# Optimization experiments

Hardware: AMD Instinct MI355X
Metric: run time of the kernel (lower is better)

## Reference

```python
import jax, jax.numpy as jnp
import numpy as np

B, S, H, NH, L, V, P = 2, 1024, 768, 12, 4, 32000, 1024
HD = H // NH  # head dim = 64; matches scale_val = hidden/num_heads


def setup_inputs() -> dict:
    key = jax.random.key(0)
    ks = jax.random.split(key, 18)
    sc = 0.02
    n = jax.random.normal
    return {
        "input_ids": jax.random.randint(ks[0], (B, S), 0, V, dtype=jnp.int32),
        "seq_mask": jnp.ones((B, S), jnp.float32),
        "bpe_emb": (n(ks[1], (V, H)) * sc).astype(jnp.float32),
        "pos_emb": (n(ks[2], (P, H)) * sc).astype(jnp.float32),
        "qkv_w": (n(ks[3], (L, H, 3 * H)) * sc).astype(jnp.float32),
        "qkv_b": jnp.zeros((L, 3 * H), jnp.float32),
        "res_w": (n(ks[4], (L, H, H)) * sc).astype(jnp.float32),
        "res_b": jnp.zeros((L, H), jnp.float32),
        "ln1_g": jnp.ones((L, H), jnp.float32),
        "ln1_b": jnp.zeros((L, H), jnp.float32),
        "ff1_w": (n(ks[5], (L, H, 4 * H)) * sc).astype(jnp.float32),
        "ff1_b": jnp.zeros((L, 4 * H), jnp.float32),
        "ff2_w": (n(ks[6], (L, 4 * H, H)) * sc).astype(jnp.float32),
        "ff2_b": jnp.zeros((L, H), jnp.float32),
        "ln2_g": jnp.ones((L, H), jnp.float32),
        "ln2_b": jnp.zeros((L, H), jnp.float32),
        "pred_w": (n(ks[7], (H, V)) * sc).astype(jnp.float32),
    }


def _layer_norm(x, g, b, e=1e-5):
    u = jnp.mean(x, -1, keepdims=True)
    s = jnp.mean((x - u) ** 2, -1, keepdims=True)
    return g * ((x - u) / jnp.sqrt(s + e)) + b


def _attention(x, seq_mask, w_qkv, b_qkv, w_res, b_res):
    qkv = x @ w_qkv + b_qkv                    # [B,S,3H]
    q, k, v = jnp.split(qkv, 3, axis=-1)
    q = q.reshape(B, S, NH, HD)
    k = k.reshape(B, S, NH, HD)
    v = v.reshape(B, S, NH, HD)
    score = jnp.einsum('bqhd,bkhd->bhqk', q, k) / jnp.sqrt(jnp.float32(HD))
    tril = jnp.tril(jnp.ones((S, S), jnp.float32))           # causal
    mask = tril[None, None] * seq_mask[:, None, None, :]      # [B,1,S,S]
    score = score + (1.0 - mask) * -1e9
    prob = jax.nn.softmax(score, axis=-1)      # dropout rate 0 -> identity
    val = jnp.einsum('bhqk,bkhd->bqhd', prob, v).reshape(B, S, H)
    return val @ w_res + b_res                 # dropout rate 0 -> identity


def reference(input_ids, seq_mask, bpe_emb, pos_emb, qkv_w, qkv_b, res_w, res_b,
              ln1_g, ln1_b, ff1_w, ff1_b, ff2_w, ff2_b, ln2_g, ln2_b, pred_w):
    pos_idx = jnp.arange(S)
    h = bpe_emb[input_ids] + pos_emb[pos_idx][None]           # [B,S,H]
    for l in range(L):
        a = _attention(h, seq_mask, qkv_w[l], qkv_b[l], res_w[l], res_b[l])
        h = _layer_norm(h + a, ln1_g[l], ln1_b[l])
        m = (jax.nn.gelu(h @ ff1_w[l] + ff1_b[l], approximate=False)
             @ ff2_w[l] + ff2_b[l])
        h = _layer_norm(h + m, ln2_g[l], ln2_b[l])
    pred_score = h @ pred_w                                   # [B,S,V]
    pred_prob = jax.nn.softmax(pred_score, axis=-1)
    return pred_score, pred_prob
```

## Files before the change

### kernel.cpp

```cpp
#include <hip/hip_runtime.h>
#include <math.h>

#define BB 2
#define SS 1024
#define HH 768
#define NHEAD 12
#define HDIM 64
#define NLAYER 4
#define VV 32000
#define MROWS (BB*SS)

typedef unsigned short u16;
typedef __attribute__((ext_vector_type(8))) short short8;
typedef __attribute__((ext_vector_type(4))) float f32x4;
typedef __attribute__((ext_vector_type(4))) unsigned short u16x4;

__device__ __forceinline__ u16 f2bf(float f) {
    union { float f; unsigned u; } x; x.f = f;
    unsigned r = (x.u + 0x7fff + ((x.u >> 16) & 1)) >> 16;
    return (u16)r;
}
__device__ __forceinline__ float bf2f(u16 b) {
    union { unsigned u; float f; } x; x.u = ((unsigned)b) << 16;
    return x.f;
}

__device__ __forceinline__ void gload_lds16(const u16* g, u16* l) {
    __builtin_amdgcn_global_load_lds((const __attribute__((address_space(1))) void*)g,
                                     (__attribute__((address_space(3))) void*)l, 16, 0, 0);
}

__global__ __launch_bounds__(256) void conv_transpose(
    const float* __restrict__ W, u16* __restrict__ Wt, int K, int N) {
    int l = blockIdx.z;
    W  += (size_t)l * K * N;
    Wt += (size_t)l * K * N;
    __shared__ u16 tile[32][33];
    int k0 = blockIdx.y * 32, n0 = blockIdx.x * 32;
    int t = threadIdx.x;
    int ky = t >> 3, nx = (t & 7) * 4;
    float4 v = *(const float4*)(W + (size_t)(k0 + ky) * N + n0 + nx);
    tile[nx + 0][ky] = f2bf(v.x);
    tile[nx + 1][ky] = f2bf(v.y);
    tile[nx + 2][ky] = f2bf(v.z);
    tile[nx + 3][ky] = f2bf(v.w);
    __syncthreads();
    int nr = t >> 3, kc = (t & 7) * 4;
    u16x4 o;
    o[0] = tile[nr][kc + 0]; o[1] = tile[nr][kc + 1];
    o[2] = tile[nr][kc + 2]; o[3] = tile[nr][kc + 3];
    *(u16x4*)(Wt + (size_t)(n0 + nr) * K + k0 + kc) = o;
}

__global__ void embed_kernel(const int* __restrict__ ids,
                             const float* __restrict__ bpe,
                             const float* __restrict__ pos,
                             float* __restrict__ h, u16* __restrict__ hb) {
    int row = blockIdx.x;
    int s = row % SS;
    int id = ids[row];
    const float4* br = (const float4*)(bpe + (size_t)id * HH);
    const float4* pr = (const float4*)(pos + (size_t)s * HH);
    float4* hr = (float4*)(h + (size_t)row * HH);
    u16x4* hbr = (u16x4*)(hb + (size_t)row * HH);
    int t = threadIdx.x;
    float4 a = br[t], c = pr[t];
    a.x += c.x; a.y += c.y; a.z += c.z; a.w += c.w;
    hr[t] = a;
    u16x4 u; u[0] = f2bf(a.x); u[1] = f2bf(a.y); u[2] = f2bf(a.z); u[3] = f2bf(a.w);
    hbr[t] = u;
}

template<int BM, int ACT, int WF32, int WBF>
__global__ __launch_bounds__(256) void mfma_gemm(
    const u16* __restrict__ A, const u16* __restrict__ Wt,
    const float* __restrict__ bias, float* __restrict__ C,
    u16* __restrict__ Cb, int M, int N, int K) {
    constexpr int MR = (BM >= 128) ? 4 : 2;
    __shared__ u16 As[2 * BM * 64];
    __shared__ u16 Bs[2 * 128 * 64];
    const int tid = threadIdx.x;
    const int lane = tid & 63;
    const int wid = tid >> 6;

    const int nwg = gridDim.x * gridDim.y;
    int id = blockIdx.x + gridDim.x * blockIdx.y;
    int id2 = (nwg & 7) ? id : ((id & 7) * (nwg >> 3) + (id >> 3));
    const int brow = (id2 % gridDim.x) * BM;
    const int bcol = (id2 / gridDim.x) * 128;

    const int wr = (wid >> 1) * (MR * 16);
    const int wc = (wid & 1) * 64;
    f32x4 acc[MR][4] = {};

    const u16* Abase = A + (size_t)brow * K;
    const u16* Bbase = Wt + (size_t)bcol * K;
    const int lrow = lane & 15;
    const int lhi = lane >> 4;

    auto stage = [&](u16* Ad, u16* Bd, int kt) {
#pragma unroll
        for (int c0 = 0; c0 < BM * 8; c0 += 256) {
            int c = c0 + tid;
            int r = c >> 3, s = c & 7;
            gload_lds16(Abase + (size_t)r * K + kt + ((s ^ (r & 7)) * 8), Ad + c * 8);
        }
#pragma unroll
        for (int c0 = 0; c0 < 1024; c0 += 256) {
            int c = c0 + tid;
            int r = c >> 3, s = c & 7;
            gload_lds16(Bbase + (size_t)r * K + kt + ((s ^ (r & 7)) * 8), Bd + c * 8);
        }
    };

    const int nt = K / 64;
    stage(As, Bs, 0);
    for (int t = 0; t < nt; ++t) {
        u16* Ac = As + (t & 1) * (BM * 64);
        u16* Bc = Bs + (t & 1) * (128 * 64);
        if (t + 1 < nt) {
            stage(As + ((t + 1) & 1) * (BM * 64),
                  Bs + ((t + 1) & 1) * (128 * 64), (t + 1) * 64);
            if constexpr (BM == 128)      asm volatile("s_waitcnt vmcnt(8)" ::: "memory");
            else                          asm volatile("s_waitcnt vmcnt(6)" ::: "memory");
        } else {
            asm volatile("s_waitcnt vmcnt(0)" ::: "memory");
        }
        __builtin_amdgcn_s_barrier();
        __builtin_amdgcn_sched_barrier(0);

        short8 a[MR][2], b[4][2];
#pragma unroll
        for (int m = 0; m < MR; ++m) {
            const int R = wr + m * 16 + lrow;
            char* rp = (char*)Ac + R * 128;
#pragma unroll
            for (int kk = 0; kk < 2; ++kk)
                a[m][kk] = *(const short8*)(rp + (((kk * 4 + lhi) ^ (R & 7)) * 16));
        }
#pragma unroll
        for (int n = 0; n < 4; ++n) {
            const int R = wc + n * 16 + lrow;
            char* rp = (char*)Bc + R * 128;
#pragma unroll
            for (int kk = 0; kk < 2; ++kk)
                b[n][kk] = *(const short8*)(rp + (((kk * 4 + lhi) ^ (R & 7)) * 16));
        }
        __builtin_amdgcn_s_setprio(1);
#pragma unroll
        for (int kk = 0; kk < 2; ++kk)
#pragma unroll
            for (int m = 0; m < MR; ++m)
#pragma unroll
                for (int n = 0; n < 4; ++n)
                    acc[m][n] = __builtin_amdgcn_mfma_f32_16x16x32_bf16(a[m][kk], b[n][kk], acc[m][n], 0, 0, 0);
        __builtin_amdgcn_s_setprio(0);

        __builtin_amdgcn_sched_barrier(0);
        __builtin_amdgcn_s_barrier();
    }

    const int lr4 = (lane >> 4) * 4;
#pragma unroll
    for (int n = 0; n < 4; ++n) {
        int col = bcol + wc + n * 16 + lrow;
        float bv = bias ? bias[col] : 0.f;
#pragma unroll
        for (int m = 0; m < MR; ++m) {
#pragma unroll
            for (int j = 0; j < 4; ++j) {
                int row = brow + wr + m * 16 + lr4 + j;
                float v = acc[m][n][j] + bv;
                if (ACT == 1) v = 0.5f * v * (1.f + erff(v * 0.70710678118654752f));
                if (WF32) C[(size_t)row * N + col] = v;
                if (WBF)  Cb[(size_t)row * N + col] = f2bf(v);
            }
        }
    }
}

__global__ __launch_bounds__(256) void attn_kernel(
    const u16* __restrict__ qkvb, const float* __restrict__ seq_mask,
    u16* __restrict__ av) {
    __shared__ u16 Ks[64 * 64];
    __shared__ u16 Vt[64 * 64];
    __shared__ u16 Ps[64 * 64];
    const int qb = gridDim.x - 1 - blockIdx.x;
    const int hd = blockIdx.y, b = blockIdx.z;
    const int t = threadIdx.x;
    const int lane = t & 63;
    const int w = t >> 6;
    const int lrow = lane & 15;
    const int lhi = lane >> 4;
    const int q0 = qb * 64;
    const size_t rs = 3 * HH;

    short8 aq[2];
    {
        const u16* qrow = qkvb + (size_t)(b * SS + q0 + w * 16 + lrow) * rs + hd * HDIM;
        aq[0] = *(const short8*)(qrow + lhi * 8);
        aq[1] = *(const short8*)(qrow + 32 + lhi * 8);
    }

    f32x4 o[4] = {};
    float m_[4] = {-INFINITY, -INFINITY, -INFINITY, -INFINITY};
    float l_[4] = {0.f, 0.f, 0.f, 0.f};

    const int kr = t >> 2, dc = t & 3;
    short8 kA, kB, vA, vB;
    {
        const u16* kbase = qkvb + (size_t)(b * SS + kr) * rs + HH + hd * HDIM + dc * 16;
        kA = *(const short8*)(kbase);
        kB = *(const short8*)(kbase + 8);
        vA = *(const short8*)(kbase + HH);
        vB = *(const short8*)(kbase + HH + 8);
    }

    for (int kt = 0; kt <= qb; ++kt) {
        const int k0 = kt * 64;
        __syncthreads();
        {
            char* krowp = (char*)Ks + kr * 128;
            *(short8*)(krowp + (((dc * 32 + 0)  ^ ((kr & 7) << 4)))) = kA;
            *(short8*)(krowp + (((dc * 32 + 16) ^ ((kr & 7) << 4)))) = kB;
#pragma unroll
            for (int e = 0; e < 8; ++e) {
                int d0 = dc * 16 + e;
                int d1 = dc * 16 + 8 + e;
                *(u16*)((char*)Vt + d0 * 128 + ((kr * 2) ^ ((d0 & 7) << 4))) = (u16)vA[e];
                *(u16*)((char*)Vt + d1 * 128 + ((kr * 2) ^ ((d1 & 7) << 4))) = (u16)vB[e];
            }
        }
        __syncthreads();

        if (kt < qb) {
            const u16* kbase = qkvb + (size_t)(b * SS + k0 + 64 + kr) * rs + HH + hd * HDIM + dc * 16;
            kA = *(const short8*)(kbase);
            kB = *(const short8*)(kbase + 8);
            vA = *(const short8*)(kbase + HH);
            vB = *(const short8*)(kbase + HH + 8);
        }

        f32x4 s[4] = {};
        __builtin_amdgcn_s_setprio(1);
#pragma unroll
        for (int n = 0; n < 4; ++n) {
            const int krow = n * 16 + lrow;
            char* kp = (char*)Ks + krow * 128;
#pragma unroll
            for (int c = 0; c < 2; ++c) {
                short8 bk = *(const short8*)(kp + ((c * 64 + lhi * 16) ^ ((krow & 7) << 4)));
                s[n] = __builtin_amdgcn_mfma_f32_16x16x32_bf16(aq[c], bk, s[n], 0, 0, 0);
            }
        }
        __builtin_amdgcn_s_setprio(0);

        float sm[4];
#pragma unroll
        for (int n = 0; n < 4; ++n) sm[n] = seq_mask[b * SS + k0 + n * 16 + lrow];
        const int diag = (kt == qb);
#pragma unroll
        for (int j = 0; j < 4; ++j) {
            const int qglob = q0 + w * 16 + lhi * 4 + j;
            float sv[4];
#pragma unroll
            for (int n = 0; n < 4; ++n) {
                const int kglob = k0 + n * 16 + lrow;
                float msk = (diag && kglob > qglob) ? 0.f : sm[n];
                sv[n] = s[n][j] * 0.125f + (1.f - msk) * (-1e9f);
            }
            float tm = fmaxf(fmaxf(sv[0], sv[1]), fmaxf(sv[2], sv[3]));
            tm = fmaxf(tm, __shfl_xor(tm, 1));
            tm = fmaxf(tm, __shfl_xor(tm, 2));
            tm = fmaxf(tm, __shfl_xor(tm, 4));
            tm = fmaxf(tm, __shfl_xor(tm, 8));
            float mn = fmaxf(m_[j], tm);
            float sc = __expf(m_[j] - mn);
            float ps = 0.f;
#pragma unroll
            for (int n = 0; n < 4; ++n) {
                float p = __expf(sv[n] - mn);
                s[n][j] = p;
                ps += p;
            }
            ps += __shfl_xor(ps, 1);
            ps += __shfl_xor(ps, 2);
            ps += __shfl_xor(ps, 4);
            ps += __shfl_xor(ps, 8);
            l_[j] = l_[j] * sc + ps;
            m_[j] = mn;
#pragma unroll
            for (int dn = 0; dn < 4; ++dn) o[dn][j] *= sc;
        }

#pragma unroll
        for (int j = 0; j < 4; ++j) {
            const int prow = w * 16 + lhi * 4 + j;
            char* pp = (char*)Ps + prow * 128;
#pragma unroll
            for (int n = 0; n < 4; ++n)
                *(u16*)(pp + ((n * 32 + lrow * 2) ^ ((prow & 7) << 4))) = f2bf(s[n][j]);
        }

        const int arow = w * 16 + lrow;
        char* ap_p = (char*)Ps + arow * 128;
        __builtin_amdgcn_s_setprio(1);
#pragma unroll
        for (int c = 0; c < 2; ++c) {
            short8 ap = *(const short8*)(ap_p + ((c * 64 + lhi * 16) ^ ((arow & 7) << 4)));
#pragma unroll
            for (int dn = 0; dn < 4; ++dn) {
                const int vrow = dn * 16 + lrow;
                short8 bv = *(const short8*)((char*)Vt + vrow * 128 +
                                             ((c * 64 + lhi * 16) ^ ((vrow & 7) << 4)));
                o[dn] = __builtin_amdgcn_mfma_f32_16x16x32_bf16(ap, bv, o[dn], 0, 0, 0);
            }
        }
        __builtin_amdgcn_s_setprio(0);
    }

#pragma unroll
    for (int j = 0; j < 4; ++j) {
        const int q = q0 + w * 16 + lhi * 4 + j;
        const float inv = 1.f / l_[j];
        u16* orow = av + (size_t)(b * SS + q) * HH + hd * HDIM;
#pragma unroll
        for (int dn = 0; dn < 4; ++dn)
            orow[dn * 16 + lrow] = f2bf(o[dn][j] * inv);
    }
}

__global__ __launch_bounds__(256) void add_ln_kernel(
    float* __restrict__ h, u16* __restrict__ hb,
    const u16* __restrict__ ab,
    const float* __restrict__ g, const float* __restrict__ bta) {
    const int row = blockIdx.x * 4 + (threadIdx.x >> 6);
    const int lane = threadIdx.x & 63;
    const size_t base = (size_t)row * HH;

    float x[12];
    float sum = 0.f;
#pragma unroll
    for (int c = 0; c < 3; ++c) {
        const int col = lane * 4 + c * 256;
        float4 hv = *(const float4*)(h + base + col);
        u16x4 av = *(const u16x4*)(ab + base + col);
        x[c*4+0] = hv.x + bf2f(av[0]);
        x[c*4+1] = hv.y + bf2f(av[1]);
        x[c*4+2] = hv.z + bf2f(av[2]);
        x[c*4+3] = hv.w + bf2f(av[3]);
        sum += x[c*4+0] + x[c*4+1] + x[c*4+2] + x[c*4+3];
    }
#pragma unroll
    for (int off = 32; off; off >>= 1) sum += __shfl_xor(sum, off);
    const float mean = sum * (1.0f / 768.0f);

    float vs = 0.f;
#pragma unroll
    for (int e = 0; e < 12; ++e) { float d = x[e] - mean; vs += d * d; }
#pragma unroll
    for (int off = 32; off; off >>= 1) vs += __shfl_xor(vs, off);
    const float inv = 1.0f / sqrtf(vs * (1.0f / 768.0f) + 1e-5f);

#pragma unroll
    for (int c = 0; c < 3; ++c) {
        const int col = lane * 4 + c * 256;
        float4 gv = *(const float4*)(g + col);
        float4 bv = *(const float4*)(bta + col);
        float y0 = gv.x * (x[c*4+0] - mean) * inv + bv.x;
        float y1 = gv.y * (x[c*4+1] - mean) * inv + bv.y;
        float y2 = gv.z * (x[c*4+2] - mean) * inv + bv.z;
        float y3 = gv.w * (x[c*4+3] - mean) * inv + bv.w;
        float4 hv; hv.x = y0; hv.y = y1; hv.z = y2; hv.w = y3;
        *(float4*)(h + base + col) = hv;
        u16x4 u; u[0] = f2bf(y0); u[1] = f2bf(y1); u[2] = f2bf(y2); u[3] = f2bf(y3);
        *(u16x4*)(hb + base + col) = u;
    }
}

__global__ __launch_bounds__(512) void softmax_v_kernel(
    const float* __restrict__ score, float* __restrict__ prob) {
    __shared__ u16 srow[VV];
    __shared__ float red[512];
    int row = blockIdx.x;
    int t = threadIdx.x;
    const float4* sr = (const float4*)(score + (size_t)row * VV);
    float4* pr = (float4*)(prob + (size_t)row * VV);
    const int n4 = VV / 4;

    float mx = -INFINITY;
    for (int i = t; i < n4; i += 512) {
        float4 v = sr[i];
        u16x4 u; u[0] = f2bf(v.x); u[1] = f2bf(v.y); u[2] = f2bf(v.z); u[3] = f2bf(v.w);
        *(u16x4*)(srow + i * 4) = u;
        mx = fmaxf(mx, fmaxf(fmaxf(bf2f(u[0]), bf2f(u[1])), fmaxf(bf2f(u[2]), bf2f(u[3]))));
    }
    red[t] = mx; __syncthreads();
    for (int o = 256; o; o >>= 1) { if (t < o) red[t] = fmaxf(red[t], red[t + o]); __syncthreads(); }
    mx = red[0];
    __syncthreads();

    float s = 0.f;
    for (int i = t; i < n4; i += 512) {
        u16x4 u = *(const u16x4*)(srow + i * 4);
        s += __expf(bf2f(u[0]) - mx) + __expf(bf2f(u[1]) - mx)
           + __expf(bf2f(u[2]) - mx) + __expf(bf2f(u[3]) - mx);
    }
    red[t] = s; __syncthreads();
    for (int o = 256; o; o >>= 1) { if (t < o) red[t] += red[t + o]; __syncthreads(); }
    float inv = 1.0f / red[0];

    for (int i = t; i < n4; i += 512) {
        u16x4 u = *(const u16x4*)(srow + i * 4);
        float4 o4;
        o4.x = __expf(bf2f(u[0]) - mx) * inv; o4.y = __expf(bf2f(u[1]) - mx) * inv;
        o4.z = __expf(bf2f(u[2]) - mx) * inv; o4.w = __expf(bf2f(u[3]) - mx) * inv;
        pr[i] = o4;
    }
}

extern "C" void kernel_launch(void* const* d_in, const int* in_sizes, int n_in,
                              void* d_out, int out_size, void* d_ws, size_t ws_size,
                              hipStream_t stream) {
    const int*   ids      = (const int*)d_in[0];
    const float* seq_mask = (const float*)d_in[1];
    const float* bpe      = (const float*)d_in[2];
    const float* pos      = (const float*)d_in[3];
    const float* qkv_w    = (const float*)d_in[4];
    const float* qkv_b    = (const float*)d_in[5];
    const float* res_w    = (const float*)d_in[6];
    const float* res_b    = (const float*)d_in[7];
    const float* ln1_g    = (const float*)d_in[8];
    const float* ln1_b    = (const float*)d_in[9];
    const float* ff1_w    = (const float*)d_in[10];
    const float* ff1_b    = (const float*)d_in[11];
    const float* ff2_w    = (const float*)d_in[12];
    const float* ff2_b    = (const float*)d_in[13];
    const float* ln2_g    = (const float*)d_in[14];
    const float* ln2_b    = (const float*)d_in[15];
    const float* pred_w   = (const float*)d_in[16];

    float* out_score = (float*)d_out;
    float* out_prob  = out_score + (size_t)MROWS * VV;

    size_t off = 0;
    auto take = [&](size_t bytes) -> size_t {
        size_t p = off; off += (bytes + 255) & ~(size_t)255; return p;
    };
    const size_t o_qkvT = take((size_t)NLAYER * HH * 3 * HH * 2);
    const size_t o_resT = take((size_t)NLAYER * HH * HH * 2);
    const size_t o_ff1T = take((size_t)NLAYER * HH * 4 * HH * 2);
    const size_t o_ff2T = take((size_t)NLAYER * 4 * HH * HH * 2);
    const size_t o_predT = take((size_t)HH * VV * 2);
    const size_t o_h    = take((size_t)MROWS * HH * 4);
    const size_t o_ab   = take((size_t)MROWS * HH * 2);
    const size_t o_qkvb = take((size_t)MROWS * 3 * HH * 2);
    const size_t o_hb   = take((size_t)MROWS * HH * 2);
    const size_t o_avb  = take((size_t)MROWS * HH * 2);
    const size_t o_midb = take((size_t)MROWS * 4 * HH * 2);
    const size_t need = off;

    char* arena = (ws_size >= need) ? (char*)d_ws : (char*)out_prob;
    u16*   qkvT = (u16*)(arena + o_qkvT);
    u16*   resT = (u16*)(arena + o_resT);
    u16*   ff1T = (u16*)(arena + o_ff1T);
    u16*   ff2T = (u16*)(arena + o_ff2T);
    u16*   predT = (u16*)(arena + o_predT);
    float* h    = (float*)(arena + o_h);
    u16*   ab   = (u16*)(arena + o_ab);
    u16*   qkvb = (u16*)(arena + o_qkvb);
    u16*   hb   = (u16*)(arena + o_hb);
    u16*   avb  = (u16*)(arena + o_avb);
    u16*   midb = (u16*)(arena + o_midb);

    conv_transpose<<<dim3(3 * HH / 32, HH / 32, NLAYER), 256, 0, stream>>>(qkv_w, qkvT, HH, 3 * HH);
    conv_transpose<<<dim3(HH / 32, HH / 32, NLAYER), 256, 0, stream>>>(res_w, resT, HH, HH);
    conv_transpose<<<dim3(4 * HH / 32, HH / 32, NLAYER), 256, 0, stream>>>(ff1_w, ff1T, HH, 4 * HH);
    conv_transpose<<<dim3(HH / 32, 4 * HH / 32, NLAYER), 256, 0, stream>>>(ff2_w, ff2T, 4 * HH, HH);
    conv_transpose<<<dim3(VV / 32, HH / 32, 1), 256, 0, stream>>>(pred_w, predT, HH, VV);

    embed_kernel<<<MROWS, 192, 0, stream>>>(ids, bpe, pos, h, hb);

    for (int l = 0; l < NLAYER; ++l) {
        mfma_gemm<64, 0, 0, 1><<<dim3(MROWS / 64, 3 * HH / 128), 256, 0, stream>>>(
            hb, qkvT + (size_t)l * HH * 3 * HH, qkv_b + (size_t)l * 3 * HH,
            nullptr, qkvb, MROWS, 3 * HH, HH);
        attn_kernel<<<dim3(SS / 64, NHEAD, BB), 256, 0, stream>>>(qkvb, seq_mask, avb);
        mfma_gemm<64, 0, 0, 1><<<dim3(MROWS / 64, HH / 128), 256, 0, stream>>>(
            avb, resT + (size_t)l * HH * HH, res_b + (size_t)l * HH,
            nullptr, ab, MROWS, HH, HH);
        add_ln_kernel<<<MROWS / 4, 256, 0, stream>>>(h, hb, ab,
            ln1_g + (size_t)l * HH, ln1_b + (size_t)l * HH);
        mfma_gemm<64, 1, 0, 1><<<dim3(MROWS / 64, 4 * HH / 128), 256, 0, stream>>>(
            hb, ff1T + (size_t)l * HH * 4 * HH, ff1_b + (size_t)l * 4 * HH,
            nullptr, midb, MROWS, 4 * HH, HH);
        mfma_gemm<64, 0, 0, 1><<<dim3(MROWS / 64, HH / 128), 256, 0, stream>>>(
            midb, ff2T + (size_t)l * 4 * HH * HH, ff2_b + (size_t)l * HH,
            nullptr, ab, MROWS, HH, 4 * HH);
        add_ln_kernel<<<MROWS / 4, 256, 0, stream>>>(h, hb, ab,
            ln2_g + (size_t)l * HH, ln2_b + (size_t)l * HH);
    }

    mfma_gemm<128, 0, 1, 0><<<dim3(MROWS / 128, VV / 128), 256, 0, stream>>>(
        hb, predT, nullptr, out_score, nullptr, MROWS, VV, HH);
    softmax_v_kernel<<<MROWS, 512, 0, stream>>>(out_score, out_prob);
}
```

Baseline: 994.8 us.

## Widen attention key tiles to 128 and merge weight transposes into one launch

```diff
diff --git a/kernel.cpp b/kernel.cpp
--- a/kernel.cpp
+++ b/kernel.cpp
@@ -30,13 +30,38 @@
                                      (__attribute__((address_space(3))) void*)l, 16, 0, 0);
 }
 
-__global__ __launch_bounds__(256) void conv_transpose(
-    const float* __restrict__ W, u16* __restrict__ Wt, int K, int N) {
-    int l = blockIdx.z;
-    W  += (size_t)l * K * N;
-    Wt += (size_t)l * K * N;
+__global__ __launch_bounds__(256) void conv_all(
+    const float* __restrict__ qkv_w, u16* __restrict__ qkvT,
+    const float* __restrict__ res_w, u16* __restrict__ resT,
+    const float* __restrict__ ff1_w, u16* __restrict__ ff1T,
+    const float* __restrict__ ff2_w, u16* __restrict__ ff2T,
+    const float* __restrict__ pred_w, u16* __restrict__ predT) {
+    int id = blockIdx.x;
+    const float* W; u16* Wt; int K, N, rem;
+    if (id < 6912) {
+        int l = id / 1728; rem = id - l * 1728;
+        W = qkv_w + (size_t)l * HH * 3 * HH; Wt = qkvT + (size_t)l * HH * 3 * HH;
+        K = HH; N = 3 * HH;
+    } else if (id < 9216) {
+        id -= 6912; int l = id / 576; rem = id - l * 576;
+        W = res_w + (size_t)l * HH * HH; Wt = resT + (size_t)l * HH * HH;
+        K = HH; N = HH;
+    } else if (id < 18432) {
+        id -= 9216; int l = id / 2304; rem = id - l * 2304;
+        W = ff1_w + (size_t)l * HH * 4 * HH; Wt = ff1T + (size_t)l * HH * 4 * HH;
+        K = HH; N = 4 * HH;
+    } else if (id < 27648) {
+        id -= 18432; int l = id / 2304; rem = id - l * 2304;
+        W = ff2_w + (size_t)l * 4 * HH * HH; Wt = ff2T + (size_t)l * 4 * HH * HH;
+        K = 4 * HH; N = HH;
+    } else {
+        rem = id - 27648;
+        W = pred_w; Wt = predT; K = HH; N = VV;
+    }
+    const int nt = N / 32;
+    const int k0 = (rem / nt) * 32, n0 = (rem % nt) * 32;
+
     __shared__ u16 tile[32][33];
-    int k0 = blockIdx.y * 32, n0 = blockIdx.x * 32;
     int t = threadIdx.x;
     int ky = t >> 3, nx = (t & 7) * 4;
     float4 v = *(const float4*)(W + (size_t)(k0 + ky) * N + n0 + nx);
@@ -182,9 +207,9 @@
 __global__ __launch_bounds__(256) void attn_kernel(
     const u16* __restrict__ qkvb, const float* __restrict__ seq_mask,
     u16* __restrict__ av) {
-    __shared__ u16 Ks[64 * 64];
-    __shared__ u16 Vt[64 * 64];
-    __shared__ u16 Ps[64 * 64];
+    __shared__ u16 Ks[128 * 64];
+    __shared__ u16 Vt[64 * 128];
+    __shared__ u16 Ps[64 * 128];
     const int qb = gridDim.x - 1 - blockIdx.x;
     const int hd = blockIdx.y, b = blockIdx.z;
     const int t = threadIdx.x;
@@ -206,70 +231,79 @@
     float m_[4] = {-INFINITY, -INFINITY, -INFINITY, -INFINITY};
     float l_[4] = {0.f, 0.f, 0.f, 0.f};
 
-    const int kr = t >> 2, dc = t & 3;
-    short8 kA, kB, vA, vB;
+    const int kr = t >> 1;
+    const int ch = t & 1;
+    const int ntile = (q0 + 64 + 127) / 128;
+
+    short8 kR[4], vR[4];
     {
-        const u16* kbase = qkvb + (size_t)(b * SS + kr) * rs + HH + hd * HDIM + dc * 16;
-        kA = *(const short8*)(kbase);
-        kB = *(const short8*)(kbase + 8);
-        vA = *(const short8*)(kbase + HH);
-        vB = *(const short8*)(kbase + HH + 8);
-    }
-
-    for (int kt = 0; kt <= qb; ++kt) {
-        const int k0 = kt * 64;
+        const u16* kbase = qkvb + (size_t)(b * SS + kr) * rs + HH + hd * HDIM + ch * 32;
+#pragma unroll
+        for (int i = 0; i < 4; ++i) {
+            kR[i] = *(const short8*)(kbase + i * 8);
+            vR[i] = *(const short8*)(kbase + HH + i * 8);
+        }
+    }
+
+    for (int kt = 0; kt < ntile; ++kt) {
+        const int k0 = kt * 128;
         __syncthreads();
         {
-            char* krowp = (char*)Ks + kr * 128;
-            *(short8*)(krowp + (((dc * 32 + 0)  ^ ((kr & 7) << 4)))) = kA;
-            *(short8*)(krowp + (((dc * 32 + 16) ^ ((kr & 7) << 4)))) = kB;
-#pragma unroll
-            for (int e = 0; e < 8; ++e) {
-                int d0 = dc * 16 + e;
-                int d1 = dc * 16 + 8 + e;
-                *(u16*)((char*)Vt + d0 * 128 + ((kr * 2) ^ ((d0 & 7) << 4))) = (u16)vA[e];
-                *(u16*)((char*)Vt + d1 * 128 + ((kr * 2) ^ ((d1 & 7) << 4))) = (u16)vB[e];
-            }
+            char* kp = (char*)Ks + kr * 128;
+#pragma unroll
+            for (int i = 0; i < 4; ++i)
+                *(short8*)(kp + (((ch * 4 + i) ^ (kr & 7)) << 4)) = kR[i];
+            const int vslot = kr >> 3;
+            const int voff = (kr & 7) * 2;
+#pragma unroll
+            for (int i = 0; i < 4; ++i)
+#pragma unroll
+                for (int e = 0; e < 8; ++e) {
+                    int d = ch * 32 + i * 8 + e;
+                    *(u16*)((char*)Vt + d * 256 + ((vslot ^ (d & 15)) << 4) + voff) = (u16)vR[i][e];
+                }
         }
         __syncthreads();
 
-        if (kt < qb) {
-            const u16* kbase = qkvb + (size_t)(b * SS + k0 + 64 + kr) * rs + HH + hd * HDIM + dc * 16;
-            kA = *(const short8*)(kbase);
-            kB = *(const short8*)(kbase + 8);
-            vA = *(const short8*)(kbase + HH);
-            vB = *(const short8*)(kbase + HH + 8);
-        }
-
-        f32x4 s[4] = {};
+        if (kt + 1 < ntile) {
+            const u16* kbase = qkvb + (size_t)(b * SS + k0 + 128 + kr) * rs + HH + hd * HDIM + ch * 32;
+#pragma unroll
+            for (int i = 0; i < 4; ++i) {
+                kR[i] = *(const short8*)(kbase + i * 8);
+                vR[i] = *(const short8*)(kbase + HH + i * 8);
+            }
+        }
+
+        f32x4 s[8] = {};
         __builtin_amdgcn_s_setprio(1);
 #pragma unroll
-        for (int n = 0; n < 4; ++n) {
+        for (int n = 0; n < 8; ++n) {
             const int krow = n * 16 + lrow;
             char* kp = (char*)Ks + krow * 128;
 #pragma unroll
             for (int c = 0; c < 2; ++c) {
-                short8 bk = *(const short8*)(kp + ((c * 64 + lhi * 16) ^ ((krow & 7) << 4)));
+                short8 bk = *(const short8*)(kp + (((c * 4 + lhi) ^ (krow & 7)) << 4));
                 s[n] = __builtin_amdgcn_mfma_f32_16x16x32_bf16(aq[c], bk, s[n], 0, 0, 0);
             }
         }
         __builtin_amdgcn_s_setprio(0);
 
-        float sm[4];
-#pragma unroll
-        for (int n = 0; n < 4; ++n) sm[n] = seq_mask[b * SS + k0 + n * 16 + lrow];
-        const int diag = (kt == qb);
+        float sm[8];
+#pragma unroll
+        for (int n = 0; n < 8; ++n) sm[n] = seq_mask[b * SS + k0 + n * 16 + lrow];
+        const int diag = (kt == ntile - 1);
 #pragma unroll
         for (int j = 0; j < 4; ++j) {
             const int qglob = q0 + w * 16 + lhi * 4 + j;
-            float sv[4];
-#pragma unroll
-            for (int n = 0; n < 4; ++n) {
+            float sv[8];
+#pragma unroll
+            for (int n = 0; n < 8; ++n) {
                 const int kglob = k0 + n * 16 + lrow;
                 float msk = (diag && kglob > qglob) ? 0.f : sm[n];
                 sv[n] = s[n][j] * 0.125f + (1.f - msk) * (-1e9f);
             }
-            float tm = fmaxf(fmaxf(sv[0], sv[1]), fmaxf(sv[2], sv[3]));
+            float tm = fmaxf(fmaxf(fmaxf(sv[0], sv[1]), fmaxf(sv[2], sv[3])),
+                             fmaxf(fmaxf(sv[4], sv[5]), fmaxf(sv[6], sv[7])));
             tm = fmaxf(tm, __shfl_xor(tm, 1));
             tm = fmaxf(tm, __shfl_xor(tm, 2));
             tm = fmaxf(tm, __shfl_xor(tm, 4));
@@ -278,7 +312,7 @@
             float sc = __expf(m_[j] - mn);
             float ps = 0.f;
 #pragma unroll
-            for (int n = 0; n < 4; ++n) {
+            for (int n = 0; n < 8; ++n) {
                 float p = __expf(sv[n] - mn);
                 s[n][j] = p;
                 ps += p;
@@ -296,23 +330,26 @@
 #pragma unroll
         for (int j = 0; j < 4; ++j) {
             const int prow = w * 16 + lhi * 4 + j;
-            char* pp = (char*)Ps + prow * 128;
-#pragma unroll
-            for (int n = 0; n < 4; ++n)
-                *(u16*)(pp + ((n * 32 + lrow * 2) ^ ((prow & 7) << 4))) = f2bf(s[n][j]);
+            char* pp = (char*)Ps + prow * 256;
+            const int poff = (lrow & 7) * 2;
+#pragma unroll
+            for (int n = 0; n < 8; ++n) {
+                int slot = 2 * n + (lrow >> 3);
+                *(u16*)(pp + ((slot ^ (prow & 15)) << 4) + poff) = f2bf(s[n][j]);
+            }
         }
 
         const int arow = w * 16 + lrow;
-        char* ap_p = (char*)Ps + arow * 128;
+        char* ap_p = (char*)Ps + arow * 256;
         __builtin_amdgcn_s_setprio(1);
 #pragma unroll
-        for (int c = 0; c < 2; ++c) {
-            short8 ap = *(const short8*)(ap_p + ((c * 64 + lhi * 16) ^ ((arow & 7) << 4)));
+        for (int c = 0; c < 4; ++c) {
+            short8 ap = *(const short8*)(ap_p + (((c * 4 + lhi) ^ (arow & 15)) << 4));
 #pragma unroll
             for (int dn = 0; dn < 4; ++dn) {
                 const int vrow = dn * 16 + lrow;
-                short8 bv = *(const short8*)((char*)Vt + vrow * 128 +
-                                             ((c * 64 + lhi * 16) ^ ((vrow & 7) << 4)));
+                short8 bv = *(const short8*)((char*)Vt + vrow * 256 +
+                                             (((c * 4 + lhi) ^ (vrow & 15)) << 4));
                 o[dn] = __builtin_amdgcn_mfma_f32_16x16x32_bf16(ap, bv, o[dn], 0, 0, 0);
             }
         }
@@ -473,11 +510,8 @@
     u16*   avb  = (u16*)(arena + o_avb);
     u16*   midb = (u16*)(arena + o_midb);
 
-    conv_transpose<<<dim3(3 * HH / 32, HH / 32, NLAYER), 256, 0, stream>>>(qkv_w, qkvT, HH, 3 * HH);
-    conv_transpose<<<dim3(HH / 32, HH / 32, NLAYER), 256, 0, stream>>>(res_w, resT, HH, HH);
-    conv_transpose<<<dim3(4 * HH / 32, HH / 32, NLAYER), 256, 0, stream>>>(ff1_w, ff1T, HH, 4 * HH);
-    conv_transpose<<<dim3(HH / 32, 4 * HH / 32, NLAYER), 256, 0, stream>>>(ff2_w, ff2T, 4 * HH, HH);
-    conv_transpose<<<dim3(VV / 32, HH / 32, 1), 256, 0, stream>>>(pred_w, predT, HH, VV);
+    conv_all<<<51648, 256, 0, stream>>>(qkv_w, qkvT, res_w, resT,
+                                        ff1_w, ff1T, ff2_w, ff2T, pred_w, predT);
 
     embed_kernel<<<MROWS, 192, 0, stream>>>(ids, bpe, pos, h, hb);
 
```

After: 959.8 us. -3.5%, faster.
